# Kernel optimization log

Hardware: AMD Instinct MI355X
Metric: run time of the kernel (lower is better)

The kernel has to match this reference:

```python
import jax, jax.numpy as jnp
import numpy as np
from jax import lax

B, L, E, R = 128, 8, 384, 500
HP, HM, HD = 4, 6, 2   # pair-encoder heads, final-mha heads, dynamic-memory heads
MAXLEN = 8
EPS = 1e-5


def _ln(x, g, b):
    m = x.mean(-1, keepdims=True)
    v = ((x - m) ** 2).mean(-1, keepdims=True)
    return (x - m) / jnp.sqrt(v + EPS) * g + b


def _gelu(x):
    return jax.nn.gelu(x, approximate=False)


def _mha(qi, ki, vi, in_w, in_b, out_w, out_b, h):
    # torch nn.MultiheadAttention with packed in_proj ([3E,E]) and out_proj
    Em = qi.shape[-1]
    dh = Em // h
    q = qi @ in_w[:Em].T + in_b[:Em]
    k = ki @ in_w[Em:2 * Em].T + in_b[Em:2 * Em]
    v = vi @ in_w[2 * Em:].T + in_b[2 * Em:]
    def sp(x):
        b_, l_, _ = x.shape
        return x.reshape(b_, l_, h, dh).transpose(0, 2, 1, 3)
    q, k, v = sp(q), sp(k), sp(v)
    a = jax.nn.softmax(jnp.einsum('bhqd,bhkd->bhqk', q, k) / jnp.sqrt(jnp.float32(dh)), axis=-1)
    o = jnp.einsum('bhqk,bhkd->bhqd', a, v).transpose(0, 2, 1, 3).reshape(qi.shape)
    return o @ out_w.T + out_b


def _forward(inputs, emb, rel_pos, qkv_dyn_w, qkv_dyn_b, out_dyn_w, out_dyn_b,
             ln_dyn_g, ln_dyn_b, conv_w, conv_b, tl_in_w, tl_in_b, tl_out_w, tl_out_b,
             tl_ln1_g, tl_ln1_b, tl_ln2_g, tl_ln2_b, tl_ff1_w, tl_ff1_b, tl_ff2_w, tl_ff2_b,
             fc_score_w, fc_score_b, fcq_w, fcq_b, fck_w, fck_b, fcv_w, fcv_b,
             mha_in_w, mha_in_b, mha_out_w, mha_out_b, lnf1_g, lnf1_b, lnf2_g, lnf2_b,
             ff1_w, ff1_b, ff2_w, ff2_b):
    # ---- update_memory: 2-head self-attention over relation embeddings ----
    rel_emb = emb[:R]                                   # [R,E]
    qkv = rel_emb @ qkv_dyn_w.T + qkv_dyn_b             # [R,3E]
    qm, km, vm = jnp.split(qkv, 3, axis=-1)
    dh = E // HD
    def sph(x):
        return x.reshape(R, HD, dh).transpose(1, 0, 2)  # [HD,R,dh]
    qm, km, vm = sph(qm), sph(km), sph(vm)
    am = jax.nn.softmax(jnp.einsum('hqd,hkd->hqk', qm, km) / jnp.sqrt(jnp.float32(dh)), axis=-1)
    om = jnp.einsum('hqk,hkd->hqd', am, vm).transpose(1, 0, 2).reshape(R, E)
    om = om @ out_dyn_w.T + out_dyn_b
    relation_mem = _ln(rel_emb + om, ln_dyn_g, ln_dyn_b)  # [R,E]

    def pair_encode(x):  # x: [N,2,E]  Conv1d(k=3,pad=1) + 2 post-norm transformer layers
        xc = lax.conv_general_dilated(x.transpose(0, 2, 1), conv_w, (1,), [(1, 1)],
                                      dimension_numbers=('NCH', 'OIH', 'NCH'))
        x = (xc + conv_b[None, :, None]).transpose(0, 2, 1)
        for l in range(2):
            a = _mha(x, x, x, tl_in_w[l], tl_in_b[l], tl_out_w[l], tl_out_b[l], HP)
            x = _ln(x + a, tl_ln1_g[l], tl_ln1_b[l])
            f = _gelu(x @ tl_ff1_w[l].T + tl_ff1_b[l]) @ tl_ff2_w[l].T + tl_ff2_b[l]
            x = _ln(x + f, tl_ln2_g[l], tl_ln2_b[l])
        return x

    def fuse(pair):  # pair: [B,1,E] -> memory_attention_fuse
        mem = jnp.concatenate([jnp.broadcast_to(relation_mem[None], (B, R, E)), pair], axis=1)
        q = pair @ fcq_w.T + fcq_b
        k = mem @ fck_w.T + fck_b
        v = mem @ fcv_w.T + fcv_b
        a = _mha(q, k, v, mha_in_w, mha_in_b, mha_out_w, mha_out_b, HM)
        x = _ln(pair + a, lnf1_g, lnf1_b)
        f = _gelu(x @ ff1_w.T + ff1_b) @ ff2_w.T + ff2_b
        return _ln(x + f, lnf2_g, lnf2_b)

    pos = jnp.minimum(jnp.arange(L), MAXLEN - 1)
    seq = emb[inputs] + rel_pos[pos]                    # [B,L,E]

    losses = []
    for _ in range(L - 1):                              # L-1 sequential reduce steps
        Lc = seq.shape[1]
        if Lc <= 2:
            losses.append(jnp.zeros((B, 1), jnp.float32))
            continue
        # all adjacent pairs at once (replaces the per-pair python loop)
        pairs = jnp.stack([seq[:, :-1], seq[:, 1:]], axis=2) + rel_pos[:2]  # [B,Lc-1,2,E]
        hid = pair_encode(pairs.reshape(B * (Lc - 1), 2, E))[:, -1, :].reshape(B, Lc - 1, E)
        sc = jax.nn.sigmoid(hid @ fc_score_w.T + fc_score_b)[..., 0]        # [B,Lc-1]
        idx = jnp.argmax(sc, axis=-1)                                       # [B]
        logp = jax.nn.log_softmax(sc, axis=-1)
        losses.append(-(jnp.exp(logp) * logp).sum(-1, keepdims=True))       # entropy [B,1]
        sel = jnp.take_along_axis(hid, idx[:, None, None], axis=1)          # [B,1,E]
        fused = fuse(sel)                                                   # [B,1,E]
        # scatter fused at idx, delete row idx+1 (compaction)
        updated = jnp.where(jnp.arange(Lc)[None, :, None] == idx[:, None, None], fused, seq)
        gidx = jnp.arange(Lc - 1)[None, :]
        gidx = gidx + (gidx >= (idx + 1)[:, None])
        seq = jnp.take_along_axis(updated, gidx[:, :, None], axis=1)        # [B,Lc-1,E]

    # ---- final memory_attention ----
    Lf = seq.shape[1]  # == 2
    mem = jnp.concatenate([jnp.broadcast_to(relation_mem[None], (B, R, E)), seq], axis=1)
    q = seq @ fcq_w.T + fcq_b
    k = mem @ fck_w.T + fck_b
    a = _mha(q, k, k, mha_in_w, mha_in_b, mha_out_w, mha_out_b, HM)
    x = _ln(seq + a, lnf1_g, lnf1_b)
    f = _gelu(x @ ff1_w.T + ff1_b) @ ff2_w.T + ff2_b
    x = _ln(x + f, lnf2_g, lnf2_b)
    logits = jnp.einsum('ble,bme->blm', x, mem) / jnp.sqrt(jnp.float32(E))
    gate = jnp.ones((R + Lf,), jnp.float32)             # gate_mask buffer is all ones
    logits = logits * gate                              # [B,Lf,R+Lf]
    logp2 = jax.nn.log_softmax(logits, axis=-1)
    ent = -(jnp.exp(logp2) * logp2).sum(-1)             # [B,Lf]
    loss = jnp.concatenate(losses + [ent], axis=-1)     # [B,L+1]
    pred = logits[:, -1, :]                             # [B,R+Lf]
    return pred, loss


def setup_inputs():
    key = jax.random.key(0)
    ctr = [0]
    def nk():
        ctr[0] += 1
        return jax.random.fold_in(key, ctr[0])
    def W(*s):
        return jax.random.normal(nk(), s, jnp.float32) * 0.02
    def Z(*s):
        return jnp.zeros(s, jnp.float32)
    def O(*s):
        return jnp.ones(s, jnp.float32)
    d = {}
    d['inputs'] = jax.random.randint(nk(), (B, L), 0, R)
    d['emb'] = W(R + 1, E).at[R].set(0.0)  # padding_idx row zero
    d['rel_pos'] = W(MAXLEN, E)
    d['qkv_dyn_w'] = W(3 * E, E); d['qkv_dyn_b'] = Z(3 * E)
    d['out_dyn_w'] = W(E, E); d['out_dyn_b'] = Z(E)
    d['ln_dyn_g'] = O(E); d['ln_dyn_b'] = Z(E)
    d['conv_w'] = W(E, E, 3); d['conv_b'] = Z(E)
    d['tl_in_w'] = W(2, 3 * E, E); d['tl_in_b'] = Z(2, 3 * E)
    d['tl_out_w'] = W(2, E, E); d['tl_out_b'] = Z(2, E)
    d['tl_ln1_g'] = O(2, E); d['tl_ln1_b'] = Z(2, E)
    d['tl_ln2_g'] = O(2, E); d['tl_ln2_b'] = Z(2, E)
    d['tl_ff1_w'] = W(2, 4 * E, E); d['tl_ff1_b'] = Z(2, 4 * E)
    d['tl_ff2_w'] = W(2, E, 4 * E); d['tl_ff2_b'] = Z(2, E)
    d['fc_score_w'] = W(1, E); d['fc_score_b'] = Z(1)
    d['fcq_w'] = W(E, E); d['fcq_b'] = Z(E)
    d['fck_w'] = W(E, E); d['fck_b'] = Z(E)
    d['fcv_w'] = W(E, E); d['fcv_b'] = Z(E)
    d['mha_in_w'] = W(3 * E, E); d['mha_in_b'] = Z(3 * E)
    d['mha_out_w'] = W(E, E); d['mha_out_b'] = Z(E)
    d['lnf1_g'] = O(E); d['lnf1_b'] = Z(E)
    d['lnf2_g'] = O(E); d['lnf2_b'] = Z(E)
    d['ff1_w'] = W(4 * E, E); d['ff1_b'] = Z(4 * E)
    d['ff2_w'] = W(E, 4 * E); d['ff2_b'] = Z(E)
    return d


def reference(inputs, emb, rel_pos, qkv_dyn_w, qkv_dyn_b, out_dyn_w, out_dyn_b,
              ln_dyn_g, ln_dyn_b, conv_w, conv_b, tl_in_w, tl_in_b, tl_out_w, tl_out_b,
              tl_ln1_g, tl_ln1_b, tl_ln2_g, tl_ln2_b, tl_ff1_w, tl_ff1_b, tl_ff2_w, tl_ff2_b,
              fc_score_w, fc_score_b, fcq_w, fcq_b, fck_w, fck_b, fcv_w, fcv_b,
              mha_in_w, mha_in_b, mha_out_w, mha_out_b, lnf1_g, lnf1_b, lnf2_g, lnf2_b,
              ff1_w, ff1_b, ff2_w, ff2_b):
    return _forward(inputs, emb, rel_pos, qkv_dyn_w, qkv_dyn_b, out_dyn_w, out_dyn_b,
                    ln_dyn_g, ln_dyn_b, conv_w, conv_b, tl_in_w, tl_in_b, tl_out_w, tl_out_b,
                    tl_ln1_g, tl_ln1_b, tl_ln2_g, tl_ln2_b, tl_ff1_w, tl_ff1_b, tl_ff2_w, tl_ff2_b,
                    fc_score_w, fc_score_b, fcq_w, fcq_b, fck_w, fck_b, fcv_w, fcv_b,
                    mha_in_w, mha_in_b, mha_out_w, mha_out_b, lnf1_g, lnf1_b, lnf2_g, lnf2_b,
                    ff1_w, ff1_b, ff2_w, ff2_b)
```

## Files before the change

kernel.cpp:

```cpp
#include <hip/hip_runtime.h>

#define CDIV(a,b) (((a)+(b)-1)/(b))

typedef __bf16 bf16x8 __attribute__((ext_vector_type(8)));
typedef float  f32x4  __attribute__((ext_vector_type(4)));
#define MFMA16(a,b,c) __builtin_amdgcn_mfma_f32_16x16x32_bf16(a,b,c,0,0,0)

__device__ __forceinline__ void ldst16(const unsigned short* g, unsigned short* l){
  __builtin_amdgcn_global_load_lds(
      (const __attribute__((address_space(1))) unsigned int*)g,
      (__attribute__((address_space(3))) unsigned int*)l, 16, 0, 0);
}

__device__ __forceinline__ float waveSum(float v){
#pragma unroll
  for(int o=32;o;o>>=1) v += __shfl_xor(v,o);
  return v;
}
__device__ __forceinline__ float waveMax(float v){
#pragma unroll
  for(int o=32;o;o>>=1) v = fmaxf(v,__shfl_xor(v,o));
  return v;
}

// ... 523 lines not shown
  for(int i=0;i<3;i++){
    int c = tid + i*128;
    float t = bias ? bias[c] : 0.f;
    const float* p = Pp + (size_t)row*384 + c;
    for(int k=0;k<KS;k++) t += p[(size_t)k*M*384];
    v[i] = x[c] + t; s += v[i];
  }
  s = waveSum(s);
  __shared__ float p1[2];
  if((tid&63)==0) p1[tid>>6]=s;
  __syncthreads();
  float mean = (p1[0]+p1[1])*(1.f/384.f);
  float vs=0.f;
#pragma unroll
  for(int i=0;i<3;i++){ float d=v[i]-mean; vs += d*d; }
  vs = waveSum(vs);
  __shared__ float p2[2];
  if((tid&63)==0) p2[tid>>6]=vs;
  __syncthreads();
  float rstd = rsqrtf((p2[0]+p2[1])*(1.f/384.f) + 1e-5f);
#pragma unroll
  for(int i=0;i<3;i++){ int c = tid + i*128; o[c] = (v[i]-mean)*rstd*g[c] + be[c]; }
}

__global__ __launch_bounds__(256)
void gemm_nn(const float* __restrict__ A, int lda,
             const float* __restrict__ Bm, int ldb,
             float* __restrict__ C, int ldc,
             int M, int N, int K, float scale)
{
  __shared__ float As[16][68];
  __shared__ float Bs[16][68];
  const int bm = blockIdx.x*64, bn = blockIdx.y*64;
  const int tid = threadIdx.x;
  const int lr = tid>>2;
  const int kq = (tid&3)<<2;
  const int kr = tid>>4;
  const int nq = (tid&15)<<2;
  const int tx = tid&15, ty = tid>>4;
  float acc[4][4] = {};
  for(int k0=0;k0<K;k0+=16){
    float4 av = make_float4(0.f,0.f,0.f,0.f), bv = make_float4(0.f,0.f,0.f,0.f);
    if(bm+lr < M && k0+kq < K) av = *reinterpret_cast<const float4*>(A + (size_t)(bm+lr)*lda + k0+kq);
    if(k0+kr < K && bn+nq < N) bv = *reinterpret_cast<const float4*>(Bm + (size_t)(k0+kr)*ldb + bn+nq);
    As[kq+0][lr]=av.x; As[kq+1][lr]=av.y; As[kq+2][lr]=av.z; As[kq+3][lr]=av.w;
    Bs[kr][nq+0]=bv.x; Bs[kr][nq+1]=bv.y; Bs[kr][nq+2]=bv.z; Bs[kr][nq+3]=bv.w;
    __syncthreads();
#pragma unroll
    for(int k=0;k<16;k++){
      float4 a4 = *reinterpret_cast<const float4*>(&As[k][ty<<2]);
      float4 b4 = *reinterpret_cast<const float4*>(&Bs[k][tx<<2]);
      float aa[4]={a4.x,a4.y,a4.z,a4.w};
      float bb[4]={b4.x,b4.y,b4.z,b4.w};
#pragma unroll
      for(int i=0;i<4;i++)
#pragma unroll
        for(int j=0;j<4;j++) acc[i][j] = fmaf(aa[i],bb[j],acc[i][j]);
    }
    __syncthreads();
  }
#pragma unroll
  for(int i=0;i<4;i++){
    int row = bm + (ty<<2) + i;
    if(row>=M) continue;
#pragma unroll
    for(int j=0;j<4;j++){
      int col = bn + (tx<<2) + j;
      if(col>=N) continue;
      C[(size_t)row*ldc+col]=acc[i][j]*scale;
    }
  }
}

__global__ __launch_bounds__(128)
void add_ln(const float* __restrict__ X, const float* __restrict__ T,
            float* __restrict__ O, const float* __restrict__ g,
            const float* __restrict__ be, int M, float* __restrict__ hid)
{
  int row = blockIdx.x;
  if(row>=M) return;
  const float* x = X + (size_t)row*384;
  const float* t = T + (size_t)row*384;
  float* o = O + (size_t)row*384;
  int tid = threadIdx.x;
  float v[3]; float s=0.f;
#pragma unroll
  for(int i=0;i<3;i++){ int c = tid + i*128; v[i] = x[c] + t[c]; s += v[i]; }
  s = waveSum(s);
  __shared__ float p1[2];
  if((tid&63)==0) p1[tid>>6]=s;
  __syncthreads();
  float mean = (p1[0]+p1[1])*(1.f/384.f);
  float vs=0.f;
#pragma unroll
  for(int i=0;i<3;i++){ float d=v[i]-mean; vs += d*d; }
  vs = waveSum(vs);
  __shared__ float p2[2];
  if((tid&63)==0) p2[tid>>6]=vs;
  __syncthreads();
  float rstd = rsqrtf((p2[0]+p2[1])*(1.f/384.f) + 1e-5f);
#pragma unroll
  for(int i=0;i<3;i++){
    int c = tid + i*128;
    float r = (v[i]-mean)*rstd*g[c] + be[c];
    o[c] = r;
    if(hid && (row&1)) hid[(size_t)(row>>1)*384 + c] = r;
  }
}

__global__ __launch_bounds__(256)
void softmax_rows(float* __restrict__ X, int ld, int cols)
{
  float* x = X + (size_t)blockIdx.x*ld;
  int tid = threadIdx.x;
  float m = -1e30f;
  for(int c=tid;c<cols;c+=256) m = fmaxf(m, x[c]);
  m = waveMax(m);
  __shared__ float sm[4];
  if((tid&63)==0) sm[tid>>6]=m;
  __syncthreads();
  m = fmaxf(fmaxf(sm[0],sm[1]),fmaxf(sm[2],sm[3]));
  float s=0.f;
  for(int c=tid;c<cols;c+=256){ float e = expf(x[c]-m); x[c]=e; s+=e; }
  s = waveSum(s);
  __shared__ float ss[4];
  if((tid&63)==0) ss[tid>>6]=s;
  __syncthreads();
  s = ss[0]+ss[1]+ss[2]+ss[3];
  float inv = 1.f/s;
  for(int c=tid;c<cols;c+=256) x[c]*=inv;
  for(int c=cols+tid;c<ld;c+=256) x[c]=0.f;
}

__global__ void prep_conv(const float* __restrict__ cw, const float* __restrict__ cb,
                          float* __restrict__ Wc, float* __restrict__ cb768){
  int gid = blockIdx.x*256+threadIdx.x;
  if(gid >= 384*384) return;
  int i = gid % 384, o = gid / 384;
  const float* w = cw + (size_t)gid*3;
  Wc[(size_t)o*768 + i]            = w[1];
  Wc[(size_t)o*768 + 384 + i]      = w[2];
  Wc[(size_t)(384+o)*768 + i]      = w[0];
  Wc[(size_t)(384+o)*768 + 384 + i]= w[1];
  if(gid < 768) cb768[gid] = cb[gid % 384];
}

__global__ void vt_k(const float* __restrict__ qkv, float* __restrict__ VT){
  int gid = blockIdx.x*256+threadIdx.x;
  if(gid >= 2*192*512) return;
  int k = gid & 511; int n = (gid>>9) % 192; int h = gid / 98304;
  VT[gid] = (k<500) ? qkv[(size_t)k*1152 + 768 + h*192 + n] : 0.f;
}

__global__ void prep_attn(const float* __restrict__ K1, const float* __restrict__ Vf,
                          const float* __restrict__ Vl, float* __restrict__ Kp,
                          float* __restrict__ VTf, float* __restrict__ VTl){
  int gid = blockIdx.x*256+threadIdx.x;
  if(gid < 196608){
    int j = gid / 384;
    Kp[gid] = (j<500) ? K1[gid] : 0.f;
    return;
  }
  int g2 = gid - 196608;
  const float* V; float* VT;
  if(g2 < 196608){ V = Vf; VT = VTf; }
  else { g2 -= 196608; if(g2 >= 196608) return; V = Vl; VT = VTl; }
  int j = g2 & 511; int d = (g2>>9) & 63; int h = g2 >> 15;
  VT[g2] = (j<500) ? V[(size_t)j*384 + h*64 + d] : 0.f;
}

__global__ void compose_bias(const float* __restrict__ inw, const float* __restrict__ inb,
                             const float* __restrict__ qb, const float* __restrict__ kb,
                             const float* __restrict__ vb, float* __restrict__ cb){
  int gid = blockIdx.x*256+threadIdx.x;
  if(gid>=1536) return;
  int seg = gid/384, i = gid%384;
  const float* wrow; const float* bsrc; float b2;
  if(seg==0){ wrow=inw + (size_t)i*384;       bsrc=qb; b2=inb[i]; }
  else if(seg==1){ wrow=inw + (size_t)(384+i)*384; bsrc=kb; b2=inb[384+i]; }
  else if(seg==2){ wrow=inw + (size_t)(768+i)*384; bsrc=vb; b2=inb[768+i]; }
  else          { wrow=inw + (size_t)(768+i)*384; bsrc=kb; b2=inb[768+i]; }
  float s=0.f;
  for(int t=0;t<384;t++) s = fmaf(wrow[t], bsrc[t], s);
  cb[gid] = s + b2;
}

#define NSEG 18
struct SplitArgs {
  const float* src[NSEG];
  unsigned short* dh[NSEG];
  unsigned short* dl[NSEG];
  int start[NSEG+1];
  int ld[NSEG];
};
__global__ void split_all(SplitArgs a){
  int gid = blockIdx.x*256+threadIdx.x;
  if(gid >= a.start[NSEG]) return;
  int s=0;
  while(s<NSEG-1 && gid >= a.start[s+1]) s++;
  int off = gid - a.start[s];
  int K = a.ld[s];
  int r = off / K, c = off - r*K;
  int dst = ((r>>6)*(K>>6) + (c>>6))*4096 + ((r&63)<<6) + ((c&63) ^ ((r&7)<<3));
  float v = a.src[s][off];
  unsigned short h = f2bf(v);
  a.dh[s][dst] = h;
  a.dl[s][dst] = f2bf(v - bf2f(h));
}

__global__ void seq_init(const int* __restrict__ inp, const float* __restrict__ emb,
                         const float* __restrict__ rp, float* __restrict__ seq){
  int gid = blockIdx.x*256+threadIdx.x;
  if(gid >= 128*8*384) return;
  int j = gid % 384; int l = (gid/384) & 7; int b = gid / 3072;
  int tok = inp[b*8 + l];
  seq[gid] = emb[(size_t)tok*384 + j] + rp[l*384 + j];
}

__global__ void build_pairs(const float* __restrict__ seq, const float* __restrict__ rp,
                            float* __restrict__ pairs, int N, int P){
  int gid = blockIdx.x*256+threadIdx.x;
  if(gid >= N*768) return;
  int c = gid % 768; int n = gid / 768;
  int t = c / 384; int j = c % 384;
  int i = n % P; int b = n / P;
  pairs[gid] = seq[((size_t)b*8 + i + t)*384 + j] + rp[t*384 + j];
}

__global__ __launch_bounds__(256)
void attn2_one(const float* __restrict__ QKV, float* __restrict__ O, int N){
  int n = blockIdx.x;
  if(n>=N) return;
  int tid = threadIdx.x, lane = tid&63, h = tid>>6;
  __shared__ float pr[4][2][2];
  const float* base = QKV + (size_t)(2*n)*1152;
  const float* q0 = base + h*96;
  const float* q1 = base + 1152 + h*96;
  const float* k0 = base + 384 + h*96;
  const float* k1 = base + 1152 + 384 + h*96;
  float q0a=q0[lane], q1a=q1[lane], k0a=k0[lane], k1a=k1[lane];
  float q0b=0.f,q1b=0.f,k0b=0.f,k1b=0.f;
  if(lane<32){ q0b=q0[64+lane]; q1b=q1[64+lane]; k0b=k0[64+lane]; k1b=k1[64+lane]; }
  float s00 = waveSum(q0a*k0a + q0b*k0b);
  float s01 = waveSum(q0a*k1a + q0b*k1b);
  float s10 = waveSum(q1a*k0a + q1b*k0b);
  float s11 = waveSum(q1a*k1a + q1b*k1b);
  if(lane==0){
    const float sc = 0.1020620726159658f;
    s00*=sc; s01*=sc; s10*=sc; s11*=sc;
    float m0=fmaxf(s00,s01); float e00=expf(s00-m0), e01=expf(s01-m0); float i0=1.f/(e00+e01);
    float m1=fmaxf(s10,s11); float e10=expf(s10-m1), e11=expf(s11-m1); float i1=1.f/(e10+e11);
    pr[h][0][0]=e00*i0; pr[h][0][1]=e01*i0;
    pr[h][1][0]=e10*i1; pr[h][1][1]=e11*i1;
  }
  __syncthreads();
  const float* v0 = base + 768;
  const float* v1 = base + 1152 + 768;
  float* o = O + (size_t)(2*n)*384;
#pragma unroll
  for(int i=0;i<3;i++){
    int c = tid + i*256;
    int t = c / 384, j = c % 384; int hh = j/96;
    o[(size_t)t*384 + j] = pr[hh][t][0]*v0[j] + pr[hh][t][1]*v1[j];
  }
}

__global__ __launch_bounds__(256)
void score_select3(float* __restrict__ hid, const float* __restrict__ xb,
                   const float* __restrict__ w, const float* __restrict__ b0,
                   int P, int* __restrict__ idxb, float* __restrict__ lossSlot,
                   float* __restrict__ sel, int doScatter){
  int b = blockIdx.x;
  int tid = threadIdx.x, lane = tid&63, wv = tid>>6;
  __shared__ float scs[8];
  __shared__ int sidx;
  if(doScatter){
    int oldIdx = idxb[b];
#pragma unroll
    for(int e=0;e<2;e++){
      int s = oldIdx-1+e; s = max(0, min(s, P-1));
      const float* src = xb + ((size_t)(2*(2*b+e)+1))*384;
      float* dst = hid + ((size_t)b*7 + s)*384;
      for(int c=tid;c<384;c+=256) dst[c] = src[c];
      __syncthreads();
    }
  }
  for(int pi=wv; pi<P; pi+=4){
    const float* x = hid + ((size_t)b*7 + pi)*384;
    float s=0.f;
#pragma unroll
    for(int i=0;i<6;i++){ int c = lane + i*64; s = fmaf(x[c], w[c], s); }
    s = waveSum(s);
    if(lane==0) scs[pi] = 1.f/(1.f+expf(-(s + b0[0])));
  }
  __syncthreads();
  if(tid==0){
    float m = scs[0]; int am = 0;
    for(int i=1;i<P;i++){ float v=scs[i]; if(v>m){m=v;am=i;} }
    float z=0.f, sx=0.f;
    for(int i=0;i<P;i++){ float e=expf(scs[i]-m); z+=e; sx=fmaf(e,scs[i],sx); }
    lossSlot[(size_t)b*9] = (m + logf(z)) - sx/z;
    idxb[b] = am;
    sidx = am;
  }
  __syncthreads();
  const float* src = hid + ((size_t)b*7 + sidx)*384;
  for(int c=tid;c<384;c+=256) sel[(size_t)b*384+c] = src[c];
}

template<int NE>
__global__ __launch_bounds__(256)
void softmax_ext2(float* __restrict__ S, const float* __restrict__ qkv1,
                  float* __restrict__ E, int R){
  int m = blockIdx.x;
  int r = m % R, h = m / R;
  int rbase = (NE==2) ? (r & ~1) : r;
  float* x = S + (size_t)m*512;
  int tid = threadIdx.x, lane = tid&63, wv = tid>>6;
  __shared__ float r4[4];
  __shared__ float exs[2];
  if(wv < NE){
    const float* q = qkv1 + (size_t)r*1152 + h*64;
    const float* k = qkv1 + (size_t)(rbase+wv)*1152 + 384 + h*64;
    float s = waveSum(q[lane]*k[lane]) * 0.125f;
    if(lane==0) exs[wv] = s;
  }
  __syncthreads();
  float mx = -1e30f;
  for(int c=tid;c<500;c+=256) mx = fmaxf(mx, x[c]);
  if(tid < NE) mx = fmaxf(mx, exs[tid]);
  mx = waveMax(mx);
  if(lane==0) r4[wv]=mx;
  __syncthreads();
  mx = fmaxf(fmaxf(r4[0],r4[1]),fmaxf(r4[2],r4[3]));
  float s=0.f;
  for(int c=tid;c<500;c+=256){ float e=expf(x[c]-mx); x[c]=e; s+=e; }
  float et=0.f;
  if(tid < NE){ et=expf(exs[tid]-mx); s+=et; }
  s = waveSum(s);
  __syncthreads();
  if(lane==0) r4[wv]=s;
  __syncthreads();
  float inv = 1.f/(r4[0]+r4[1]+r4[2]+r4[3]);
  for(int c=tid;c<500;c+=256) x[c]*=inv;
  if(tid < NE) E[(size_t)m*NE+tid] = et*inv;
}

template<int NE>
__global__ void pv_epi2(const float* __restrict__ Pp, const float* __restrict__ E,
                        const float* __restrict__ qkv, float* __restrict__ O, int R){
  int gid = blockIdx.x*256+threadIdx.x;
  if(gid >= R*384) return;
  int r = gid / 384; int c = gid % 384; int h = c >> 6; int d = c & 63;
  int m = h*R + r;
  int rbase = (NE==2) ? (r & ~1) : r;
  const float* p = Pp + ((size_t)(h*8)*R + r)*64 + d;
  float v = 0.f;
#pragma unroll
  for(int k=0;k<8;k++) v += p[(size_t)k*R*64];
#pragma unroll
  for(int e=0;e<NE;e++)
    v = fmaf(E[(size_t)m*NE+e], qkv[(size_t)(rbase+e)*1152 + 768 + c], v);
  O[gid] = v;
}

__global__ void merge_all(const float* __restrict__ seqOld, const float* __restrict__ fused,
                          const float* __restrict__ hidOld, const float* __restrict__ rp,
                          const int* __restrict__ idxb,
                          float* __restrict__ seqNew, float* __restrict__ hidNew,
                          float* __restrict__ pairs, int P, int last){
  int gid = blockIdx.x*256+threadIdx.x;
  int nA = 128*P*384;
  if(gid < nA){
    int j = gid % 384; int rest = gid / 384; int i = rest % P; int b = rest / P;
    int id = idxb[b];
    float v = (i==id) ? fused[(size_t)b*384+j]
                      : seqOld[((size_t)b*8 + i + (i>id?1:0))*384 + j];
    seqNew[((size_t)b*8+i)*384+j] = v;
    return;
  }
  if(last) return;
  gid -= nA;
  int Pn = P-1;
  int nB = 128*Pn*384;
  if(gid < nB){
    int j = gid % 384; int rest = gid / 384; int i = rest % Pn; int b = rest / Pn;
    int idx = idxb[b];
    int si = i + (i>=idx ? 1 : 0);
    hidNew[((size_t)b*7+i)*384+j] = hidOld[((size_t)b*7+si)*384+j];
    return;
  }
  gid -= nB;
  if(gid >= 256*768) return;
  int c = gid % 768; int rr = gid / 768; int b = rr>>1; int e = rr&1;
  int idx = idxb[b];
  int s = idx-1+e; s = max(0, min(s, Pn-1));
  int t = c/384, j = c%384;
  int row = s+t;
  float v = (row==idx) ? fused[(size_t)b*384+j]
                       : seqOld[((size_t)b*8 + row + (row>idx?1:0))*384 + j];
  pairs[gid] = v + rp[t*384+j];
}

__global__ void compact_seq(const float* __restrict__ seq, float* __restrict__ out,
                            float* __restrict__ lossBase){
  int gid = blockIdx.x*256+threadIdx.x;
  if(gid < 128) lossBase[(size_t)gid*9 + 6] = 0.f;
  if(gid >= 256*384) return;
  int j = gid % 384; int r = gid / 384; int b = r>>1; int t = r&1;
  out[gid] = seq[((size_t)b*8 + t)*384 + j];
}

__global__ void logits_k(const float* __restrict__ x2, const float* __restrict__ relmem,
                         const float* __restrict__ seqf, float* __restrict__ out){
  int gid = blockIdx.x*256+threadIdx.x;
  if(gid >= 256*502) return;
  int m = gid % 502; int bt = gid / 502; int b = bt>>1;
  const float* x = x2 + (size_t)bt*384;
  const float* mr = (m<500) ? relmem + (size_t)m*384 : seqf + ((size_t)b*2 + (m-500))*384;
  float s=0.f;
#pragma unroll 8
  for(int d=0;d<384;d++) s = fmaf(x[d], mr[d], s);
  out[gid] = s * 0.05103103630798288f;
}

__global__ void pred_copy(const float* __restrict__ logits, float* __restrict__ out){
  int gid = blockIdx.x*256+threadIdx.x;
  if(gid >= 128*502) return;
  int m = gid % 502; int b = gid / 502;
  out[gid] = logits[((size_t)b*2+1)*502 + m];
}

__global__ __launch_bounds__(256)
void final_ent(const float* __restrict__ L2, float* __restrict__ lossBase){
  int row = blockIdx.x;
  const float* x = L2 + (size_t)row*502;
  int tid = threadIdx.x;
  float m = -1e30f;
  for(int c=tid;c<502;c+=256) m = fmaxf(m, x[c]);
  m = waveMax(m);
  __shared__ float sm[4];
  if((tid&63)==0) sm[tid>>6]=m;
  __syncthreads();
  m = fmaxf(fmaxf(sm[0],sm[1]),fmaxf(sm[2],sm[3]));
  float s=0.f, sx=0.f;
  for(int c=tid;c<502;c+=256){ float e=expf(x[c]-m); s+=e; sx=fmaf(e,x[c],sx); }
  s = waveSum(s); sx = waveSum(sx);
  __shared__ float ps[4], px[4];
  if((tid&63)==0){ ps[tid>>6]=s; px[tid>>6]=sx; }
  __syncthreads();
  if(tid==0){
    float S = ps[0]+ps[1]+ps[2]+ps[3];
    float SX = px[0]+px[1]+px[2]+px[3];
    float ent = (m + logf(S)) - SX/S;
    int b = row>>1, t = row&1;
    lossBase[(size_t)b*9 + 7 + t] = ent;
  }
}

extern "C" void kernel_launch(void* const* d_in, const int* in_sizes, int n_in,
                              void* d_out, int out_size, void* d_ws, size_t ws_size,
                              hipStream_t stream){
  (void)in_sizes; (void)n_in; (void)out_size; (void)ws_size;
  const int*   inputs    = (const int*)  d_in[0];
  const float* emb       = (const float*)d_in[1];
  const float* rel_pos   = (const float*)d_in[2];
  const float* qkv_dyn_w = (const float*)d_in[3];
  const float* qkv_dyn_b = (const float*)d_in[4];
  const float* out_dyn_w = (const float*)d_in[5];
  const float* out_dyn_b = (const float*)d_in[6];
  const float* ln_dyn_g  = (const float*)d_in[7];
  const float* ln_dyn_b  = (const float*)d_in[8];
  const float* conv_w    = (const float*)d_in[9];
  const float* conv_b    = (const float*)d_in[10];
  const float* tl_in_w   = (const float*)d_in[11];
  const float* tl_in_b   = (const float*)d_in[12];
  const float* tl_out_w  = (const float*)d_in[13];
  const float* tl_out_b  = (const float*)d_in[14];
  const float* tl_ln1_g  = (const float*)d_in[15];
  const float* tl_ln1_b  = (const float*)d_in[16];
  const float* tl_ln2_g  = (const float*)d_in[17];
  const float* tl_ln2_b  = (const float*)d_in[18];
  const float* tl_ff1_w  = (const float*)d_in[19];
  const float* tl_ff1_b  = (const float*)d_in[20];
  const float* tl_ff2_w  = (const float*)d_in[21];
  const float* tl_ff2_b  = (const float*)d_in[22];
  const float* fc_score_w= (const float*)d_in[23];
  const float* fc_score_b= (const float*)d_in[24];
  const float* fcq_w     = (const float*)d_in[25];
  const float* fcq_b     = (const float*)d_in[26];
  const float* fck_w     = (const float*)d_in[27];
  const float* fck_b     = (const float*)d_in[28];
  const float* fcv_w     = (const float*)d_in[29];
  const float* fcv_b     = (const float*)d_in[30];
  const float* mha_in_w  = (const float*)d_in[31];
  const float* mha_in_b  = (const float*)d_in[32];
  const float* mha_out_w = (const float*)d_in[33];
  const float* mha_out_b = (const float*)d_in[34];
  const float* lnf1_g    = (const float*)d_in[35];
  const float* lnf1_b    = (const float*)d_in[36];
  const float* lnf2_g    = (const float*)d_in[37];
  const float* lnf2_b    = (const float*)d_in[38];
  const float* ff1_w     = (const float*)d_in[39];
  const float* ff1_b     = (const float*)d_in[40];
  const float* ff2_w     = (const float*)d_in[41];
  const float* ff2_b     = (const float*)d_in[42];

  float* ws = (float*)d_ws;
  size_t off = 0;
  auto Aa = [&](size_t n){ float* p = ws + off; off += n; return p; };
  float* relmem = Aa(192000);
  float* K1mem  = Aa(192000);
  float* V1f    = Aa(192000);
  float* V1l    = Aa(192000);
  float* K1padf = Aa(196608);
  float* VT1f   = Aa(196608);
  float* VT1lf  = Aa(196608);
  float* cb     = Aa(1536);
  float* cb768  = Aa(768);
  float* seqA_  = Aa(393216);
  float* seqB_  = Aa(393216);
  float* hidA_  = Aa(344064);
  float* hidB_  = Aa(344064);
  float* fqkv1  = Aa(147456);
  float* gqkv1  = Aa(294912);
  unsigned short* SH = (unsigned short*)Aa(3514368);
  unsigned short* SL = (unsigned short*)Aa(3514368);
  float* Pp     = Aa(2359296);
  float* pairs  = Aa(688128);
  float* xbuf   = Aa(688128);
  float* qkvbuf = Aa(2064384);
  float* obuf   = Aa(688128);
  float* tmpb   = Aa(688128);
  float* ffbuf  = Aa(2752512);
  float* probs2 = Aa(14336);
  int*   idxb   = (int*)Aa(128);
  float* sel    = Aa(49152);
  float* fo     = Aa(49152);
  float* fxf    = Aa(49152);
  float* ffused = Aa(49152);
  float* fffb   = Aa(196608);

  float* sc512   = ffbuf;
  float* Cfuse3f = ffbuf + 600000;
  float* Cvkf    = ffbuf + 1100000;
  float* Wconvf  = ffbuf + 1300000;
  float* VT      = tmpb;
  float* Sbuf = ffbuf;
  float* Ebuf = probs2;
  float* seqf = pairs;
  float* go   = obuf;
  float* gx1  = obuf + 196608;
  float* gx2  = obuf + 294912;
  float* logitsb = qkvbuf;

  float* lossBase = (float*)d_out + 128*502;

  const int o_qkvdyn=0, o_outdyn=442368, o_wconv=589824,
            o_tlin0=1179648, o_tlin1=1622016, o_tlout0=2064384, o_tlout1=2211840,
            o_tlff1_0=2359296, o_tlff1_1=2949120, o_tlff2_0=3538944, o_tlff2_1=4128768,
            o_mhaout=4718592, o_ff1=4866048, o_ff2=5455872, o_cfuse=6045696, o_cvk=6488064,
            o_vtf=6635520, o_vtl=6832128;
  const int split_total = 7028736;

  const float s192 = 0.07216878364870322f;

  gemm3<0><<<dim3(8,18),256,0,stream>>>(emb,384, qkv_dyn_w,384, qkvbuf,1152, qkv_dyn_b, 500,1152,384, 1.f);
  for(int h=0;h<2;h++)
    gemm3<0><<<dim3(8,8),256,0,stream>>>(qkvbuf + h*192,1152, qkvbuf + 384 + h*192,1152,
           sc512 + (size_t)h*256000,512, nullptr, 500,512,192, s192);
  softmax_rows<<<1000,256,0,stream>>>(sc512, 512, 500);
  vt_k<<<CDIV(2*192*512,256),256,0,stream>>>(qkvbuf, VT);
  for(int h=0;h<2;h++)
    gemm3<0><<<dim3(8,3),256,0,stream>>>(sc512 + (size_t)h*256000,512, VT + h*98304,512,
           obuf + h*192,384, nullptr, 500,192,512, 1.f);
  gemm3<0><<<dim3(8,6),256,0,stream>>>(obuf,384, out_dyn_w,384, xbuf,384, out_dyn_b, 500,384,384, 1.f);
  add_ln<<<500,128,0,stream>>>(emb, xbuf, relmem, ln_dyn_g, ln_dyn_b, 500, nullptr);

  gemm_nn<<<dim3(6,6),256,0,stream>>>(mha_in_w,384,            fcq_w,384, Cfuse3f,384,          384,384,384, 1.f);
  gemm_nn<<<dim3(6,6),256,0,stream>>>(mha_in_w + 384*384,384,  fck_w,384, Cfuse3f + 147456,384, 384,384,384, 1.f);
  gemm_nn<<<dim3(6,6),256,0,stream>>>(mha_in_w + 768*384,384,  fcv_w,384, Cfuse3f + 294912,384, 384,384,384, 1.f);
  gemm_nn<<<dim3(6,6),256,0,stream>>>(mha_in_w + 768*384,384,  fck_w,384, Cvkf,384,             384,384,384, 1.f);
  compose_bias<<<6,256,0,stream>>>(mha_in_w, mha_in_b, fcq_b, fck_b, fcv_b, cb);

  gemm3<0><<<dim3(8,6),256,0,stream>>>(relmem,384, Cfuse3f + 147456,384, K1mem,384, cb+384,  500,384,384, 1.f);
  gemm3<0><<<dim3(8,6),256,0,stream>>>(relmem,384, Cfuse3f + 294912,384, V1f,384,   cb+768,  500,384,384, 1.f);
  gemm3<0><<<dim3(8,6),256,0,stream>>>(relmem,384, Cvkf,384,            V1l,384,   cb+1152, 500,384,384, 1.f);
  prep_attn<<<CDIV(3*196608,256),256,0,stream>>>(K1mem, V1f, V1l, K1padf, VT1f, VT1lf);

  prep_conv<<<CDIV(384*384,256),256,0,stream>>>(conv_w, conv_b, Wconvf, cb768);

  {
    SplitArgs a;
    const float* srcs[NSEG] = { qkv_dyn_w, out_dyn_w, Wconvf, tl_in_w, tl_in_w + 442368,
                                tl_out_w, tl_out_w + 147456, tl_ff1_w, tl_ff1_w + 589824,
                                tl_ff2_w, tl_ff2_w + 589824, mha_out_w, ff1_w, ff2_w,
                                Cfuse3f, Cvkf, VT1f, VT1lf };
    const int offs[NSEG+1] = { o_qkvdyn, o_outdyn, o_wconv, o_tlin0, o_tlin1, o_tlout0, o_tlout1,
                               o_tlff1_0, o_tlff1_1, o_tlff2_0, o_tlff2_1, o_mhaout, o_ff1, o_ff2,
                               o_cfuse, o_cvk, o_vtf, o_vtl, split_total };
    const int lds[NSEG] = { 384, 384, 768, 384, 384, 384, 384, 384, 384,
                            1536, 1536, 384, 384, 1536, 384, 384, 512, 512 };
    for(int s=0;s<NSEG;s++){
      a.src[s]=srcs[s]; a.dh[s]=SH+offs[s]; a.dl[s]=SL+offs[s]; a.start[s]=offs[s];
      a.ld[s]=lds[s];
    }
    a.start[NSEG]=split_total;
    split_all<<<CDIV(split_total,256),256,0,stream>>>(a);
  }
  seq_init<<<CDIV(128*8*384,256),256,0,stream>>>(inputs, emb, rel_pos, seqA_);

  float* seqCur = seqA_; float* seqNxt = seqB_;
  float* hidCur = hidA_; float* hidNxt = hidB_;

  for(int it=0; it<6; ++it){
    int P = 7 - it;
    if(it == 0){
      int N = 128*7, R2 = 2*N;
      build_pairs<<<CDIV(N*768,256),256,0,stream>>>(seqCur, rel_pos, pairs, N, 7);
      gemm3s<0><<<dim3(N/64,12),256,0,stream>>>(pairs,768, SH+o_wconv,SL+o_wconv,768,
                                                xbuf,768, cb768, N,768,768);
      for(int l=0;l<2;l++){
        int oin  = l? o_tlin1  : o_tlin0;
        int oout = l? o_tlout1 : o_tlout0;
        int of1  = l? o_tlff1_1: o_tlff1_0;
        int of2  = l? o_tlff2_1: o_tlff2_0;
        gemm3s<0><<<dim3(R2/64,18),256,0,stream>>>(xbuf,384, SH+oin,SL+oin,384,
                                                   qkvbuf,1152, tl_in_b + l*1152, R2,1152,384);
        attn2_one<<<N,256,0,stream>>>(qkvbuf, obuf, N);
        gemm3s<0><<<dim3(R2/64,6),256,0,stream>>>(obuf,384, SH+oout,SL+oout,384,
                                                  tmpb,384, tl_out_b + l*384, R2,384,384);
        add_ln<<<R2,128,0,stream>>>(xbuf, tmpb, xbuf, tl_ln1_g + l*384, tl_ln1_b + l*384, R2, nullptr);
        gemm3s<1><<<dim3(R2/64,24),256,0,stream>>>(xbuf,384, SH+of1,SL+of1,384,
                                                   ffbuf,1536, tl_ff1_b + l*1536, R2,1536,384);
        gemm3s<0><<<dim3(R2/64,6),256,0,stream>>>(ffbuf,1536, SH+of2,SL+of2,1536,
                                                  tmpb,384, tl_ff2_b + l*384, R2,384,1536);
        add_ln<<<R2,128,0,stream>>>(xbuf, tmpb, xbuf, tl_ln2_g + l*384, tl_ln2_b + l*384, R2,
                                    (l==1) ? hidCur : nullptr);
      }
    } else {
      const int N2 = 256, R2 = 512;
      gemm3bk<<<dim3(4,12,12),256,0,stream>>>(pairs,768,0, SH+o_wconv,SL+o_wconv,768,0,
                                              Pp, N2,768,64,12);
      reduce_k<0><<<CDIV(N2*768,256),256,0,stream>>>(Pp, xbuf, cb768, N2*768,768,768,0,12,1, 1.f);
      for(int l=0;l<2;l++){
        int oin  = l? o_tlin1  : o_tlin0;
        int oout = l? o_tlout1 : o_tlout0;
        int of1  = l? o_tlff1_1: o_tlff1_0;
        int of2  = l? o_tlff2_1: o_tlff2_0;
        gemm3s<0><<<dim3(R2/64,18),256,0,stream>>>(xbuf,384, SH+oin,SL+oin,384,
                                                   qkvbuf,1152, tl_in_b + l*1152, R2,1152,384);
        attn2_one<<<N2,256,0,stream>>>(qkvbuf, obuf, N2);
        gemm3bk<<<dim3(R2/64,6,6),256,0,stream>>>(obuf,384,0, SH+oout,SL+oout,384,0,
                                                  Pp, R2,384,64,6);
        reduce_ln<<<R2,128,0,stream>>>(Pp, xbuf, xbuf, tl_ln1_g + l*384, tl_ln1_b + l*384,
                                       tl_out_b + l*384, R2, 6);
        gemm3s<1><<<dim3(R2/64,24),256,0,stream>>>(xbuf,384, SH+of1,SL+of1,384,
                                                   ffbuf,1536, tl_ff1_b + l*1536, R2,1536,384);
        gemm3bk<<<dim3(R2/64,6,8),256,0,stream>>>(ffbuf,1536,0, SH+of2,SL+of2,1536,0,
                                                  Pp, R2,384,192,8);
        reduce_ln<<<R2,128,0,stream>>>(Pp, xbuf, xbuf, tl_ln2_g + l*384, tl_ln2_b + l*384,
                                       tl_ff2_b + l*384, R2, 8);
      }
    }
    score_select3<<<128,256,0,stream>>>(hidCur, xbuf, fc_score_w, fc_score_b, P, idxb,
                                        lossBase + it, sel, (it>0) ? 1 : 0);
    gemm3bk<<<dim3(2,18,6),256,0,stream>>>(sel,384,0, SH+o_cfuse,SL+o_cfuse,384,0,
                                           Pp, 128,1152,64,6);
    reduce_k<0><<<CDIV(128*1152,256),256,0,stream>>>(Pp, fqkv1, cb, 128*1152,1152,1152,0,6,1, 1.f);
    gemm3z<<<dim3(2,8,6),256,0,stream>>>(fqkv1,1152,64, K1padf,384,64,
                                         Sbuf,512,128*512, 128,512,64, 0.125f);
    softmax_ext2<1><<<768,256,0,stream>>>(Sbuf, fqkv1, Ebuf, 128);
    gemm3bk<<<dim3(2,1,48),256,0,stream>>>(Sbuf,512,65536, SH+o_vtf,SL+o_vtf,512,32768,
                                           Pp, 128,64,64,8);
    pv_epi2<1><<<CDIV(128*384,256),256,0,stream>>>(Pp, Ebuf, fqkv1, fo, 128);
    gemm3bk<<<dim3(2,6,6),256,0,stream>>>(fo,384,0, SH+o_mhaout,SL+o_mhaout,384,0,
                                          Pp, 128,384,64,6);
    reduce_ln<<<128,128,0,stream>>>(Pp, sel, fxf, lnf1_g, lnf1_b, mha_out_b, 128, 6);
    gemm3bk<<<dim3(2,24,6),256,0,stream>>>(fxf,384,0, SH+o_ff1,SL+o_ff1,384,0,
                                           Pp, 128,1536,64,6);
    reduce_k<1><<<CDIV(128*1536,256),256,0,stream>>>(Pp, fffb, ff1_b, 128*1536,1536,1536,0,6,1, 1.f);
    gemm3bk<<<dim3(2,6,24),256,0,stream>>>(fffb,1536,0, SH+o_ff2,SL+o_ff2,1536,0,
                                           Pp, 128,384,64,24);
    reduce_ln<<<128,128,0,stream>>>(Pp, fxf, ffused, lnf2_g, lnf2_b, ff2_b, 128, 24);
    {
      int last = (it==5) ? 1 : 0;
      int total = 128*P*384 + (last ? 0 : (128*(P-1)*384 + 256*768));
      merge_all<<<CDIV(total,256),256,0,stream>>>(seqCur, ffused, hidCur, rel_pos, idxb,
                                                  seqNxt, hidNxt, pairs, P, last);
    }
    float* t1 = seqCur; seqCur = seqNxt; seqNxt = t1;
    float* t2 = hidCur; hidCur = hidNxt; hidNxt = t2;
  }

  compact_seq<<<CDIV(256*384,256),256,0,stream>>>(seqCur, seqf, lossBase);
  gemm3bk<<<dim3(4,12,6),256,0,stream>>>(seqf,384,0, SH+o_cfuse,SL+o_cfuse,384,0,
                                         Pp, 256,768,64,6);
  reduce_k<0><<<CDIV(256*768,256),256,0,stream>>>(Pp, gqkv1, cb, 256*768,768,1152,0,6,1, 1.f);
  gemm3bk<<<dim3(4,6,6),256,0,stream>>>(seqf,384,0, SH+o_cvk,SL+o_cvk,384,0,
                                        Pp, 256,384,64,6);
  reduce_k<0><<<CDIV(256*384,256),256,0,stream>>>(Pp, gqkv1+768, cb+1152, 256*384,384,1152,0,6,1, 1.f);
  gemm3z<<<dim3(4,8,6),256,0,stream>>>(gqkv1,1152,64, K1padf,384,64,
                                       Sbuf,512,256*512, 256,512,64, 0.125f);
  softmax_ext2<2><<<1536,256,0,stream>>>(Sbuf, gqkv1, Ebuf, 256);
  gemm3bk<<<dim3(4,1,48),256,0,stream>>>(Sbuf,512,131072, SH+o_vtl,SL+o_vtl,512,32768,
                                         Pp, 256,64,64,8);
  pv_epi2<2><<<CDIV(256*384,256),256,0,stream>>>(Pp, Ebuf, gqkv1, go, 256);
  gemm3bk<<<dim3(4,6,6),256,0,stream>>>(go,384,0, SH+o_mhaout,SL+o_mhaout,384,0,
                                        Pp, 256,384,64,6);
  reduce_ln<<<256,128,0,stream>>>(Pp, seqf, gx1, lnf1_g, lnf1_b, mha_out_b, 256, 6);
  gemm3bk<<<dim3(4,24,6),256,0,stream>>>(gx1,384,0, SH+o_ff1,SL+o_ff1,384,0,
                                         Pp, 256,1536,64,6);
  reduce_k<1><<<CDIV(256*1536,256),256,0,stream>>>(Pp, ffbuf, ff1_b, 256*1536,1536,1536,0,6,1, 1.f);
  gemm3bk<<<dim3(4,6,24),256,0,stream>>>(ffbuf,1536,0, SH+o_ff2,SL+o_ff2,1536,0,
                                         Pp, 256,384,64,24);
  reduce_ln<<<256,128,0,stream>>>(Pp, gx1, gx2, lnf2_g, lnf2_b, ff2_b, 256, 24);
  logits_k<<<CDIV(256*502,256),256,0,stream>>>(gx2, relmem, seqf, logitsb);
  pred_copy<<<CDIV(128*502,256),256,0,stream>>>(logitsb, (float*)d_out);
  final_ent<<<256,256,0,stream>>>(logitsb, lossBase);
}
```

Measured before the change: 1.712 ms.

## Fuse softmax, PV product and epilogue into one attention tail kernel

Replaces the softmax kernel, the split-bf16 MFMA PV GEMM and the PV epilogue with a single per-row kernel. It keeps probabilities in LDS and does the P·V reduction in fp32 directly against V, which removes the transposed-V preparation and its bf16 split segments. It also folds the final sequence compaction into the last merge and the prediction copy into the final entropy kernel, cutting several launches. The fused PV loop is scalar FMA per block and may make less use of the matrix units, trading GEMM throughput for fewer launches and less intermediate traffic.

Result: slower. 1.877 ms (+9.7%).

```diff
diff --git a/kernel.cpp b/kernel.cpp
--- a/kernel.cpp
+++ b/kernel.cpp
@@ -699,21 +699,11 @@
   VT[gid] = (k<500) ? qkv[(size_t)k*1152 + 768 + h*192 + n] : 0.f;
 }
 
-__global__ void prep_attn(const float* __restrict__ K1, const float* __restrict__ Vf,
-                          const float* __restrict__ Vl, float* __restrict__ Kp,
-                          float* __restrict__ VTf, float* __restrict__ VTl){
+__global__ void pad_k1(const float* __restrict__ K1, float* __restrict__ Kp){
   int gid = blockIdx.x*256+threadIdx.x;
-  if(gid < 196608){
-    int j = gid / 384;
-    Kp[gid] = (j<500) ? K1[gid] : 0.f;
-    return;
-  }
-  int g2 = gid - 196608;
-  const float* V; float* VT;
-  if(g2 < 196608){ V = Vf; VT = VTf; }
-  else { g2 -= 196608; if(g2 >= 196608) return; V = Vl; VT = VTl; }
-  int j = g2 & 511; int d = (g2>>9) & 63; int h = g2 >> 15;
-  VT[g2] = (j<500) ? V[(size_t)j*384 + h*64 + d] : 0.f;
+  if(gid >= 512*384) return;
+  int j = gid / 384;
+  Kp[gid] = (j<500) ? K1[gid] : 0.f;
 }
 
 __global__ void compose_bias(const float* __restrict__ inw, const float* __restrict__ inb,
@@ -732,7 +722,7 @@
   cb[gid] = s + b2;
 }
 
-#define NSEG 18
+#define NSEG 16
 struct SplitArgs {
   const float* src[NSEG];
   unsigned short* dh[NSEG];
@@ -857,15 +847,18 @@
 
 template<int NE>
 __global__ __launch_bounds__(256)
-void softmax_ext2(float* __restrict__ S, const float* __restrict__ qkv1,
-                  float* __restrict__ E, int R){
+void attn_tail(const float* __restrict__ S, const float* __restrict__ qkv1,
+               const float* __restrict__ V1, float* __restrict__ O, int R){
   int m = blockIdx.x;
   int r = m % R, h = m / R;
   int rbase = (NE==2) ? (r & ~1) : r;
-  float* x = S + (size_t)m*512;
+  const float* x = S + (size_t)m*512;
   int tid = threadIdx.x, lane = tid&63, wv = tid>>6;
+  __shared__ float pr[500];
   __shared__ float r4[4];
   __shared__ float exs[2];
+  __shared__ float red[4][64];
+  for(int c=tid;c<500;c+=256) pr[c] = x[c];
   if(wv < NE){
     const float* q = qkv1 + (size_t)r*1152 + h*64;
     const float* k = qkv1 + (size_t)(rbase+wv)*1152 + 384 + h*64;
@@ -874,56 +867,49 @@
   }
   __syncthreads();
   float mx = -1e30f;
-  for(int c=tid;c<500;c+=256) mx = fmaxf(mx, x[c]);
+  for(int c=tid;c<500;c+=256) mx = fmaxf(mx, pr[c]);
   if(tid < NE) mx = fmaxf(mx, exs[tid]);
   mx = waveMax(mx);
   if(lane==0) r4[wv]=mx;
   __syncthreads();
   mx = fmaxf(fmaxf(r4[0],r4[1]),fmaxf(r4[2],r4[3]));
   float s=0.f;
-  for(int c=tid;c<500;c+=256){ float e=expf(x[c]-mx); x[c]=e; s+=e; }
-  float et=0.f;
-  if(tid < NE){ et=expf(exs[tid]-mx); s+=et; }
+  for(int c=tid;c<500;c+=256){ float e=expf(pr[c]-mx); pr[c]=e; s+=e; }
+  if(tid < NE) s += expf(exs[tid]-mx);
   s = waveSum(s);
   __syncthreads();
   if(lane==0) r4[wv]=s;
   __syncthreads();
   float inv = 1.f/(r4[0]+r4[1]+r4[2]+r4[3]);
-  for(int c=tid;c<500;c+=256) x[c]*=inv;
-  if(tid < NE) E[(size_t)m*NE+tid] = et*inv;
-}
-
-template<int NE>
-__global__ void pv_epi2(const float* __restrict__ Pp, const float* __restrict__ E,
-                        const float* __restrict__ qkv, float* __restrict__ O, int R){
-  int gid = blockIdx.x*256+threadIdx.x;
-  if(gid >= R*384) return;
-  int r = gid / 384; int c = gid % 384; int h = c >> 6; int d = c & 63;
-  int m = h*R + r;
-  int rbase = (NE==2) ? (r & ~1) : r;
-  const float* p = Pp + ((size_t)(h*8)*R + r)*64 + d;
-  float v = 0.f;
-#pragma unroll
-  for(int k=0;k<8;k++) v += p[(size_t)k*R*64];
-#pragma unroll
-  for(int e=0;e<NE;e++)
-    v = fmaf(E[(size_t)m*NE+e], qkv[(size_t)(rbase+e)*1152 + 768 + c], v);
-  O[gid] = v;
+  const float* Vh = V1 + h*64;
+  float acc = 0.f;
+  for(int j=wv;j<500;j+=4) acc = fmaf(pr[j], Vh[(size_t)j*384 + lane], acc);
+  red[wv][lane] = acc;
+  __syncthreads();
+  if(wv==0){
+    float v = red[0][lane]+red[1][lane]+red[2][lane]+red[3][lane];
+#pragma unroll
+    for(int e=0;e<NE;e++)
+      v = fmaf(expf(exs[e]-mx), qkv1[(size_t)(rbase+e)*1152 + 768 + h*64 + lane], v);
+    O[(size_t)r*384 + h*64 + lane] = v*inv;
+  }
 }
 
 __global__ void merge_all(const float* __restrict__ seqOld, const float* __restrict__ fused,
                           const float* __restrict__ hidOld, const float* __restrict__ rp,
                           const int* __restrict__ idxb,
                           float* __restrict__ seqNew, float* __restrict__ hidNew,
-                          float* __restrict__ pairs, int P, int last){
+                          float* __restrict__ pairs, int P, int last, int seqLd,
+                          float* __restrict__ lossBase){
   int gid = blockIdx.x*256+threadIdx.x;
+  if(last && gid < 128) lossBase[(size_t)gid*9 + 6] = 0.f;
   int nA = 128*P*384;
   if(gid < nA){
     int j = gid % 384; int rest = gid / 384; int i = rest % P; int b = rest / P;
     int id = idxb[b];
     float v = (i==id) ? fused[(size_t)b*384+j]
                       : seqOld[((size_t)b*8 + i + (i>id?1:0))*384 + j];
-    seqNew[((size_t)b*8+i)*384+j] = v;
+    seqNew[((size_t)b*seqLd+i)*384+j] = v;
     return;
   }
   if(last) return;
@@ -947,15 +933,6 @@
   float v = (row==idx) ? fused[(size_t)b*384+j]
                        : seqOld[((size_t)b*8 + row + (row>idx?1:0))*384 + j];
   pairs[gid] = v + rp[t*384+j];
-}
-
-__global__ void compact_seq(const float* __restrict__ seq, float* __restrict__ out,
-                            float* __restrict__ lossBase){
-  int gid = blockIdx.x*256+threadIdx.x;
-  if(gid < 128) lossBase[(size_t)gid*9 + 6] = 0.f;
-  if(gid >= 256*384) return;
-  int j = gid % 384; int r = gid / 384; int b = r>>1; int t = r&1;
-  out[gid] = seq[((size_t)b*8 + t)*384 + j];
 }
 
 __global__ void logits_k(const float* __restrict__ x2, const float* __restrict__ relmem,
@@ -971,18 +948,16 @@
   out[gid] = s * 0.05103103630798288f;
 }
 
-__global__ void pred_copy(const float* __restrict__ logits, float* __restrict__ out){
-  int gid = blockIdx.x*256+threadIdx.x;
-  if(gid >= 128*502) return;
-  int m = gid % 502; int b = gid / 502;
-  out[gid] = logits[((size_t)b*2+1)*502 + m];
-}
-
 __global__ __launch_bounds__(256)
-void final_ent(const float* __restrict__ L2, float* __restrict__ lossBase){
+void final_out(const float* __restrict__ L2, float* __restrict__ lossBase,
+               float* __restrict__ pred){
   int row = blockIdx.x;
   const float* x = L2 + (size_t)row*502;
   int tid = threadIdx.x;
+  if(row & 1){
+    float* p = pred + (size_t)(row>>1)*502;
+    for(int c=tid;c<502;c+=256) p[c] = x[c];
+  }
   float m = -1e30f;
   for(int c=tid;c<502;c+=256) m = fmaxf(m, x[c]);
   m = waveMax(m);
@@ -1061,8 +1036,6 @@
   float* V1f    = Aa(192000);
   float* V1l    = Aa(192000);
   float* K1padf = Aa(196608);
-  float* VT1f   = Aa(196608);
-  float* VT1lf  = Aa(196608);
   float* cb     = Aa(1536);
   float* cb768  = Aa(768);
   float* seqA_  = Aa(393216);
@@ -1071,8 +1044,8 @@
   float* hidB_  = Aa(344064);
   float* fqkv1  = Aa(147456);
   float* gqkv1  = Aa(294912);
-  unsigned short* SH = (unsigned short*)Aa(3514368);
-  unsigned short* SL = (unsigned short*)Aa(3514368);
+  unsigned short* SH = (unsigned short*)Aa(3317760);
+  unsigned short* SL = (unsigned short*)Aa(3317760);
   float* Pp     = Aa(2359296);
   float* pairs  = Aa(688128);
   float* xbuf   = Aa(688128);
@@ -1094,7 +1067,6 @@
   float* Wconvf  = ffbuf + 1300000;
   float* VT      = tmpb;
   float* Sbuf = ffbuf;
-  float* Ebuf = probs2;
   float* seqf = pairs;
   float* go   = obuf;
   float* gx1  = obuf + 196608;
@@ -1106,9 +1078,8 @@
   const int o_qkvdyn=0, o_outdyn=442368, o_wconv=589824,
             o_tlin0=1179648, o_tlin1=1622016, o_tlout0=2064384, o_tlout1=2211840,
             o_tlff1_0=2359296, o_tlff1_1=2949120, o_tlff2_0=3538944, o_tlff2_1=4128768,
-            o_mhaout=4718592, o_ff1=4866048, o_ff2=5455872, o_cfuse=6045696, o_cvk=6488064,
-            o_vtf=6635520, o_vtl=6832128;
-  const int split_total = 7028736;
+            o_mhaout=4718592, o_ff1=4866048, o_ff2=5455872, o_cfuse=6045696, o_cvk=6488064;
+  const int split_total = 6635520;
 
   const float s192 = 0.07216878364870322f;
 
@@ -1133,7 +1104,7 @@
   gemm3<0><<<dim3(8,6),256,0,stream>>>(relmem,384, Cfuse3f + 147456,384, K1mem,384, cb+384,  500,384,384, 1.f);
   gemm3<0><<<dim3(8,6),256,0,stream>>>(relmem,384, Cfuse3f + 294912,384, V1f,384,   cb+768,  500,384,384, 1.f);
   gemm3<0><<<dim3(8,6),256,0,stream>>>(relmem,384, Cvkf,384,            V1l,384,   cb+1152, 500,384,384, 1.f);
-  prep_attn<<<CDIV(3*196608,256),256,0,stream>>>(K1mem, V1f, V1l, K1padf, VT1f, VT1lf);
+  pad_k1<<<CDIV(512*384,256),256,0,stream>>>(K1mem, K1padf);
 
   prep_conv<<<CDIV(384*384,256),256,0,stream>>>(conv_w, conv_b, Wconvf, cb768);
 
@@ -1142,12 +1113,12 @@
     const float* srcs[NSEG] = { qkv_dyn_w, out_dyn_w, Wconvf, tl_in_w, tl_in_w + 442368,
                                 tl_out_w, tl_out_w + 147456, tl_ff1_w, tl_ff1_w + 589824,
                                 tl_ff2_w, tl_ff2_w + 589824, mha_out_w, ff1_w, ff2_w,
-                                Cfuse3f, Cvkf, VT1f, VT1lf };
+                                Cfuse3f, Cvkf };
     const int offs[NSEG+1] = { o_qkvdyn, o_outdyn, o_wconv, o_tlin0, o_tlin1, o_tlout0, o_tlout1,
                                o_tlff1_0, o_tlff1_1, o_tlff2_0, o_tlff2_1, o_mhaout, o_ff1, o_ff2,
-                               o_cfuse, o_cvk, o_vtf, o_vtl, split_total };
+                               o_cfuse, o_cvk, split_total };
     const int lds[NSEG] = { 384, 384, 768, 384, 384, 384, 384, 384, 384,
-                            1536, 1536, 384, 384, 1536, 384, 384, 512, 512 };
+                            1536, 1536, 384, 384, 1536, 384, 384 };
     for(int s=0;s<NSEG;s++){
       a.src[s]=srcs[s]; a.dh[s]=SH+offs[s]; a.dl[s]=SL+offs[s]; a.start[s]=offs[s];
       a.ld[s]=lds[s];
@@ -1217,10 +1188,7 @@
     reduce_k<0><<<CDIV(128*1152,256),256,0,stream>>>(Pp, fqkv1, cb, 128*1152,1152,1152,0,6,1, 1.f);
     gemm3z<<<dim3(2,8,6),256,0,stream>>>(fqkv1,1152,64, K1padf,384,64,
                                          Sbuf,512,128*512, 128,512,64, 0.125f);
-    softmax_ext2<1><<<768,256,0,stream>>>(Sbuf, fqkv1, Ebuf, 128);
-    gemm3bk<<<dim3(2,1,48),256,0,stream>>>(Sbuf,512,65536, SH+o_vtf,SL+o_vtf,512,32768,
-                                           Pp, 128,64,64,8);
-    pv_epi2<1><<<CDIV(128*384,256),256,0,stream>>>(Pp, Ebuf, fqkv1, fo, 128);
+    attn_tail<1><<<768,256,0,stream>>>(Sbuf, fqkv1, V1f, fo, 128);
     gemm3bk<<<dim3(2,6,6),256,0,stream>>>(fo,384,0, SH+o_mhaout,SL+o_mhaout,384,0,
                                           Pp, 128,384,64,6);
     reduce_ln<<<128,128,0,stream>>>(Pp, sel, fxf, lnf1_g, lnf1_b, mha_out_b, 128, 6);
@@ -1230,17 +1198,19 @@
     gemm3bk<<<dim3(2,6,24),256,0,stream>>>(fffb,1536,0, SH+o_ff2,SL+o_ff2,1536,0,
                                            Pp, 128,384,64,24);
     reduce_ln<<<128,128,0,stream>>>(Pp, fxf, ffused, lnf2_g, lnf2_b, ff2_b, 128, 24);
-    {
-      int last = (it==5) ? 1 : 0;
-      int total = 128*P*384 + (last ? 0 : (128*(P-1)*384 + 256*768));
+    if(it < 5){
+      int total = 128*P*384 + 128*(P-1)*384 + 256*768;
       merge_all<<<CDIV(total,256),256,0,stream>>>(seqCur, ffused, hidCur, rel_pos, idxb,
-                                                  seqNxt, hidNxt, pairs, P, last);
-    }
-    float* t1 = seqCur; seqCur = seqNxt; seqNxt = t1;
-    float* t2 = hidCur; hidCur = hidNxt; hidNxt = t2;
-  }
-
-  compact_seq<<<CDIV(256*384,256),256,0,stream>>>(seqCur, seqf, lossBase);
+                                                  seqNxt, hidNxt, pairs, P, 0, 8, lossBase);
+      float* t1 = seqCur; seqCur = seqNxt; seqNxt = t1;
+      float* t2 = hidCur; hidCur = hidNxt; hidNxt = t2;
+    } else {
+      int total = 128*P*384;
+      merge_all<<<CDIV(total,256),256,0,stream>>>(seqCur, ffused, hidCur, rel_pos, idxb,
+                                                  seqf, hidNxt, pairs, P, 1, 2, lossBase);
+    }
+  }
+
   gemm3bk<<<dim3(4,12,6),256,0,stream>>>(seqf,384,0, SH+o_cfuse,SL+o_cfuse,384,0,
                                          Pp, 256,768,64,6);
   reduce_k<0><<<CDIV(256*768,256),256,0,stream>>>(Pp, gqkv1, cb, 256*768,768,1152,0,6,1, 1.f);
@@ -1249,10 +1219,7 @@
   reduce_k<0><<<CDIV(256*384,256),256,0,stream>>>(Pp, gqkv1+768, cb+1152, 256*384,384,1152,0,6,1, 1.f);
   gemm3z<<<dim3(4,8,6),256,0,stream>>>(gqkv1,1152,64, K1padf,384,64,
                                        Sbuf,512,256*512, 256,512,64, 0.125f);
-  softmax_ext2<2><<<1536,256,0,stream>>>(Sbuf, gqkv1, Ebuf, 256);
-  gemm3bk<<<dim3(4,1,48),256,0,stream>>>(Sbuf,512,131072, SH+o_vtl,SL+o_vtl,512,32768,
-                                         Pp, 256,64,64,8);
-  pv_epi2<2><<<CDIV(256*384,256),256,0,stream>>>(Pp, Ebuf, gqkv1, go, 256);
+  attn_tail<2><<<1536,256,0,stream>>>(Sbuf, gqkv1, V1l, go, 256);
   gemm3bk<<<dim3(4,6,6),256,0,stream>>>(go,384,0, SH+o_mhaout,SL+o_mhaout,384,0,
                                         Pp, 256,384,64,6);
   reduce_ln<<<256,128,0,stream>>>(Pp, seqf, gx1, lnf1_g, lnf1_b, mha_out_b, 256, 6);
@@ -1263,6 +1230,5 @@
                                          Pp, 256,384,64,24);
   reduce_ln<<<256,128,0,stream>>>(Pp, gx1, gx2, lnf2_g, lnf2_b, ff2_b, 256, 24);
   logits_k<<<CDIV(256*502,256),256,0,stream>>>(gx2, relmem, seqf, logitsb);
-  pred_copy<<<CDIV(128*502,256),256,0,stream>>>(logitsb, (float*)d_out);
-  final_ent<<<256,256,0,stream>>>(logitsb, lossBase);
-}
+  final_out<<<256,256,0,stream>>>(logitsb, lossBase, (float*)d_out);
+}
```
